# Kernel tuning notes

Measured on AMD Instinct MI355X. Metric: run time of the kernel, lower is better.

Reference implementation:

```python
import jax, jax.numpy as jnp
import numpy as np
from math import sqrt

D_MODEL = 1024
N_HEADS = 16
D_KEYS = 64
D_LLM = 4096
B, L, N = 8, 512, 1000


def _init_params(key):
    ks = jax.random.split(key, 20)
    s = 0.02
    def lin(k, din, dout):
        return jax.random.normal(k, (din, dout), jnp.float32) * s
    p = {}
    for i, pre in enumerate(('t', 'd')):
        o = i * 8
        p[pre + '_Wq'] = lin(ks[o + 0], D_MODEL, N_HEADS * D_KEYS)
        p[pre + '_bq'] = jnp.zeros((N_HEADS * D_KEYS,), jnp.float32)
        p[pre + '_Wk'] = lin(ks[o + 1], D_LLM, N_HEADS * D_KEYS)
        p[pre + '_bk'] = jnp.zeros((N_HEADS * D_KEYS,), jnp.float32)
        p[pre + '_Wv'] = lin(ks[o + 2], D_LLM, N_HEADS * D_KEYS)
        p[pre + '_bv'] = jnp.zeros((N_HEADS * D_KEYS,), jnp.float32)
        p[pre + '_Wo'] = lin(ks[o + 3], N_HEADS * D_KEYS, D_LLM)
        p[pre + '_bo'] = jnp.zeros((D_LLM,), jnp.float32)
    # adaptive fusion gate MLP: Linear(2d->d), ReLU, Linear(d->1), Sigmoid
    p['g_W1'] = jax.random.normal(ks[16], (2 * D_MODEL, D_MODEL), jnp.float32) * sqrt(2.0 / (2 * D_MODEL))
    p['g_b1'] = jnp.zeros((D_MODEL,), jnp.float32)
    p['g_W2'] = jax.random.normal(ks[17], (D_MODEL, 1), jnp.float32) * s
    p['g_b2'] = jnp.zeros((1,), jnp.float32)  # gate_bias_init = 0.0
    return p


def setup_inputs() -> dict:
    key = jax.random.key(0)
    k1, k2, k3, k4, kp = jax.random.split(key, 5)
    inp = {
        'trend_embedding': jax.random.normal(k1, (B, L, D_MODEL), jnp.float32),
        'detail_embedding': jax.random.normal(k2, (B, L, D_MODEL), jnp.float32),
        'trend_prototypes': jax.random.normal(k3, (N, D_LLM), jnp.float32),
        'detail_prototypes': jax.random.normal(k4, (N, D_LLM), jnp.float32),
    }
    inp.update(_init_params(kp))
    return inp


def _reprogram(x, protos, Wq, bq, Wk, bk, Wv, bv, Wo, bo):
    # x: (B,L,d_model), protos: (S,d_llm)
    b, l, _ = x.shape
    s = protos.shape[0]
    q = (x @ Wq + bq).reshape(b, l, N_HEADS, D_KEYS)
    k = (protos @ Wk + bk).reshape(s, N_HEADS, D_KEYS)
    v = (protos @ Wv + bv).reshape(s, N_HEADS, D_KEYS)
    scale = 1.0 / sqrt(D_KEYS)
    scores = jnp.einsum('blhe,she->bhls', q, k)  # (B,H,L,S)
    A = jax.nn.softmax(scale * scores, axis=-1)  # dropout is eval-mode identity
    out = jnp.einsum('bhls,she->blhe', A, v).reshape(b, l, N_HEADS * D_KEYS)
    return out @ Wo + bo  # (B,L,d_llm)


def reference(trend_embedding, detail_embedding, trend_prototypes, detail_prototypes,
              t_Wq, t_bq, t_Wk, t_bk, t_Wv, t_bv, t_Wo, t_bo,
              d_Wq, d_bq, d_Wk, d_bk, d_Wv, d_bv, d_Wo, d_bo,
              g_W1, g_b1, g_W2, g_b2):
    sem_trend = _reprogram(trend_embedding, trend_prototypes,
                           t_Wq, t_bq, t_Wk, t_bk, t_Wv, t_bv, t_Wo, t_bo)
    sem_detail = _reprogram(detail_embedding, detail_prototypes,
                            d_Wq, d_bq, d_Wk, d_bk, d_Wv, d_bv, d_Wo, d_bo)
    # adaptive gate from raw embeddings
    combined = jnp.concatenate([trend_embedding, detail_embedding], axis=-1)
    h = jax.nn.relu(combined @ g_W1 + g_b1)
    gate = jax.nn.sigmoid(h @ g_W2 + g_b2)  # (B,L,1)
    return gate * sem_trend + (1.0 - gate) * sem_detail
```

## Files before the change

### kernel.cpp

```cpp
#include <hip/hip_runtime.h>

typedef unsigned short u16;
typedef unsigned int u32;
typedef __attribute__((ext_vector_type(4))) u16 u16x4;
typedef __attribute__((ext_vector_type(8))) u16 u16x8;
typedef __attribute__((ext_vector_type(4))) float f32x4;
typedef __attribute__((ext_vector_type(8))) __bf16 bf16x8;

#define DEV static __device__ __forceinline__

DEV u16 f2bf(float f) {
    u32 u = __builtin_bit_cast(u32, f);
    return (u16)((u + 0x7FFFu + ((u >> 16) & 1u)) >> 16);
}
DEV float bf2f(u16 h) { return __builtin_bit_cast(float, (u32)h << 16); }

DEV f32x4 mfma16(u16x8 a, u16x8 b, f32x4 c) {
    return __builtin_amdgcn_mfma_f32_16x16x32_bf16(
        __builtin_bit_cast(bf16x8, a), __builtin_bit_cast(bf16x8, b), c, 0, 0, 0);
}

DEV void gload16(const void* g, void* l) {
    __builtin_amdgcn_global_load_lds(
        (const __attribute__((address_space(1))) void*)g,
        (__attribute__((address_space(3))) void*)l, 16, 0, 0);
}


__global__ __launch_bounds__(256) void k_build_xcomb(
    const float* __restrict__ tr, const float* __restrict__ de, u16* __restrict__ out) {
    int i = blockIdx.x * 256 + threadIdx.x;
    int m = i >> 9;
    int c = (i & 511) * 4;
    const float* src = (c < 1024) ? (tr + (size_t)m * 1024 + c)
                                  : (de + (size_t)m * 1024 + (c - 1024));
    f32x4 v = *(const f32x4*)src;
    u16x4 o = { f2bf(v[0]), f2bf(v[1]), f2bf(v[2]), f2bf(v[3]) };
    *(u16x4*)(out + (size_t)m * 2048 + c) = o;
}

__global__ __launch_bounds__(256) void k_convert(
    const float* __restrict__ in, u16* __restrict__ out, int n4) {
    int i = blockIdx.x * 256 + threadIdx.x;
    if (i >= n4) return;
    f32x4 v = ((const f32x4*)in)[i];
    u16x4 o = { f2bf(v[0]), f2bf(v[1]), f2bf(v[2]), f2bf(v[3]) };
    ((u16x4*)out)[i] = o;
}


__global__ void k_transpose_f2b(const float* __restrict__ in, u16* __restrict__ out,
                                int R, int C, int ldo) {
    __shared__ float t[32][33];
    int c0 = blockIdx.x * 32, r0 = blockIdx.y * 32;
    int tx = threadIdx.x, ty = threadIdx.y;
#pragma unroll
    for (int j = 0; j < 4; j++)
        t[ty + j * 8][tx] = in[(size_t)(r0 + ty + j * 8) * C + c0 + tx];
    __syncthreads();
#pragma unroll
    for (int j = 0; j < 4; j++)
        out[(size_t)(c0 + ty + j * 8) * ldo + r0 + tx] = f2bf(t[tx][ty + j * 8]);
}

__global__ void k_transpose_b2b(const u16* __restrict__ in, int ldi,
                                u16* __restrict__ out, int ldo, int R, int C) {
    __shared__ u16 t[32][33];
    int c0 = blockIdx.x * 32, r0 = blockIdx.y * 32;
    int tx = threadIdx.x, ty = threadIdx.y;
#pragma unroll
    for (int j = 0; j < 4; j++)
        t[ty + j * 8][tx] = in[(size_t)(r0 + ty + j * 8) * ldi + c0 + tx];
    __syncthreads();
#pragma unroll
    for (int j = 0; j < 4; j++)
        out[(size_t)(c0 + ty + j * 8) * ldo + r0 + tx] = t[tx][ty + j * 8];
}

#define MODE_BF16 0
#define MODE_BF16_RELU 1

struct GemmArgs {
    const u16* A[3];
    const u16* B[3];
    u16* o[3];
    const float* bias1[3];
    const float* bias2[3];
    int K[3];
    int lda[3];
    int ldc[3];
    int mode[3];
};

__global__ __launch_bounds__(256) void k_gemm128(GemmArgs ga) {
    __shared__ u16 As[128 * 32];
    __shared__ u16 Bs[128 * 32];
    const int z = blockIdx.z;
    const u16* A = ga.A[z];
    const u16* Bt = ga.B[z];
    u16* outp = ga.o[z];
    const float* bias1 = ga.bias1[z];
    const float* bias2 = ga.bias2[z];
    const int K = ga.K[z], lda = ga.lda[z], ldc = ga.ldc[z], mode = ga.mode[z];

    const int tid = threadIdx.x, lane = tid & 63, wid = tid >> 6;
    const int l16 = lane & 15, l4 = lane >> 4;
    const int n0 = blockIdx.x * 128, m0 = blockIdx.y * 128;
    const int wm = (wid >> 1) * 64, wn = (wid & 1) * 64;

    const int srow = wid * 32 + (lane >> 2);
    const int scol = (lane & 3) * 8;
    const u16* gA = A + (size_t)(m0 + srow) * lda + scol;
    const u16* gB = Bt + (size_t)(n0 + srow) * (size_t)K + scol;
    u16* lA = As + wid * 32 * 32;
    u16* lB = Bs + wid * 32 * 32;

    f32x4 acc[4][4] = {};

    for (int k0 = 0; k0 < K; k0 += 32) {
        gload16(gA, lA);
        gload16(gA + (size_t)16 * lda, lA + 16 * 32);
        gload16(gB, lB);
        gload16(gB + (size_t)16 * K, lB + 16 * 32);
        gA += 32;
        gB += 32;
        __syncthreads();
        u16x8 af[4], bfr[4];
#pragma unroll
        for (int m = 0; m < 4; m++) af[m] = *(const u16x8*)&As[(wm + m * 16 + l16) * 32 + l4 * 8];
#pragma unroll
        for (int n = 0; n < 4; n++) bfr[n] = *(const u16x8*)&Bs[(wn + n * 16 + l16) * 32 + l4 * 8];
#pragma unroll
        for (int m = 0; m < 4; m++)
#pragma unroll
            for (int n = 0; n < 4; n++)
                acc[m][n] = mfma16(af[m], bfr[n], acc[m][n]);
        __syncthreads();
    }

#pragma unroll
    for (int m = 0; m < 4; m++) {
#pragma unroll
        for (int n = 0; n < 4; n++) {
            int col = n0 + wn + n * 16 + l16;
#pragma unroll
            for (int j = 0; j < 4; j++) {
                int row = m0 + wm + m * 16 + l4 * 4 + j;
                float v = acc[m][n][j];
                float bb = (bias2 != nullptr && col >= 1024) ? bias2[col - 1024] : bias1[col];
                v += bb;
                if (mode == MODE_BF16_RELU) v = fmaxf(v, 0.f);
                outp[(size_t)row * ldc + col] = f2bf(v);
            }
        }
    }
}

__global__ __launch_bounds__(512, 2) void k_gemm256g(
    const u16* __restrict__ A, int ldaE,
    const u16* __restrict__ Bt, int ldbE,
    int K,
    float* __restrict__ C, int ldcE,
    const float* __restrict__ bias1, const float* __restrict__ bias2,
    const float* __restrict__ gate) {
    __shared__ __attribute__((aligned(16))) u16 sm[2 * 32768];
    char* smc = (char*)sm;

    const int tid = threadIdx.x, lane = tid & 63, wid = tid >> 6;
    const int l16 = lane & 15, l4 = lane >> 4;
    const int wm = (wid >> 2) * 128;
    const int wn = (wid & 3) * 64;
    const int m0 = blockIdx.y * 256, n0 = blockIdx.x * 256;

    const int p0 = wid * 1024 + lane * 16;
    const int p1 = p0 + 8192;
    const int rr0 = p0 >> 7, rr1 = p1 >> 7;
    const int cb0 = (p0 & 127) ^ ((rr0 & 7) << 4);
    const int cb1 = (p1 & 127) ^ ((rr1 & 7) << 4);
    const size_t ldaB = (size_t)ldaE * 2, ldbB = (size_t)ldbE * 2;
    const char* Ab = (const char*)A;
    const char* Bb = (const char*)Bt;
    const size_t aOff0 = (size_t)(m0 + rr0) * ldaB + cb0;
    const size_t aOff1 = (size_t)(m0 + rr1) * ldaB + cb1;
    const size_t bOff0 = (size_t)(n0 + rr0) * ldbB + cb0;
    const size_t bOff1 = (size_t)(n0 + rr1) * ldbB + cb1;

    auto stageA = [&](int T, int h) {
        size_t tOff = (size_t)T * 128 + (size_t)h * 128 * ldaB;
        char* d = smc + (T & 1) * 65536 + h * 16384 + wid * 1024;
        gload16(Ab + aOff0 + tOff, d);
        gload16(Ab + aOff1 + tOff, d + 8192);
    };
    auto stageB = [&](int T, int h) {
        size_t tOff = (size_t)T * 128 + (size_t)h * 128 * ldbB;
        char* d = smc + (T & 1) * 65536 + 32768 + h * 16384 + wid * 1024;
        gload16(Bb + bOff0 + tOff, d);
        gload16(Bb + bOff1 + tOff, d + 8192);
    };
    auto readA = [&](int buf, int mf, int kc) -> u16x8 {
        int row = wm + mf * 16 + l16;
        int cb = (kc * 64 + l4 * 16) ^ ((l16 & 7) << 4);
        return *(const u16x8*)(smc + buf * 65536 + row * 128 + cb);
    };
    auto readB = [&](int buf, int nf, int kc) -> u16x8 {
        int row = wn + nf * 16 + l16;
        int cb = (kc * 64 + l4 * 16) ^ ((l16 & 7) << 4);
        return *(const u16x8*)(smc + buf * 65536 + 32768 + row * 128 + cb);
    };

    f32x4 acc[8][4] = {};
    const int NT = K >> 6;

    stageA(0, 0); stageA(0, 1);
    stageB(0, 0); stageB(0, 1);
    stageB(1, 0); stageB(1, 1);
    asm volatile("s_waitcnt vmcnt(4)" ::: "memory");
    __builtin_amdgcn_s_barrier();

    for (int t = 0; t < NT; ++t) {
        const int buf = t & 1;
        u16x8 bfr[4][2];
#pragma unroll
        for (int q = 0; q < 4; ++q) {
            u16x8 af[2][2];
            if (q == 0) {
#pragma unroll
                for (int nf = 0; nf < 4; nf++)
#pragma unroll
                    for (int kc = 0; kc < 2; kc++) bfr[nf][kc] = readB(buf, nf, kc);
            }
#pragma unroll
            for (int im = 0; im < 2; im++)
#pragma unroll
                for (int kc = 0; kc < 2; kc++) af[im][kc] = readA(buf, 2 * q + im, kc);

            if (q == 0) { if (t + 1 < NT) stageA(t + 1, 0); }
            else if (q == 1) { if (t + 1 < NT) stageA(t + 1, 1); }
            else if (q == 2) { if (t + 2 < NT) stageB(t + 2, 0); }
            else { if (t + 2 < NT) stageB(t + 2, 1); }

            asm volatile("" ::: "memory");
            __builtin_amdgcn_s_barrier();
            __builtin_amdgcn_s_setprio(1);
#pragma unroll
            for (int im = 0; im < 2; im++)
#pragma unroll
                for (int nf = 0; nf < 4; nf++)
#pragma unroll
                    for (int kc = 0; kc < 2; kc++)
                        acc[2 * q + im][nf] = mfma16(af[im][kc], bfr[nf][kc], acc[2 * q + im][nf]);
            __builtin_amdgcn_s_setprio(0);
            asm volatile("" ::: "memory");
            if (q == 3) {
                if (t + 2 < NT) asm volatile("s_waitcnt vmcnt(4)" ::: "memory");
                else            asm volatile("s_waitcnt vmcnt(0)" ::: "memory");
            }
            __builtin_amdgcn_s_barrier();
        }
    }

#pragma unroll
    for (int mf = 0; mf < 8; mf++) {
#pragma unroll
        for (int j = 0; j < 4; j++) {
            int row = m0 + wm + mf * 16 + l4 * 4 + j;
            float g = gate[row];
#pragma unroll
            for (int nf = 0; nf < 4; nf++) {
                int col = n0 + wn + nf * 16 + l16;
                C[(size_t)row * ldcE + col] =
                    acc[mf][nf][j] + g * bias1[col] + (1.f - g) * bias2[col];
            }
        }
    }
}

__global__ __launch_bounds__(256) void k_gate(const u16* __restrict__ h,
                                              const float* __restrict__ W2,
                                              const float* __restrict__ b2,
                                              float* __restrict__ gate) {
    int row = blockIdx.x * 4 + (threadIdx.x >> 6);
    int lane = threadIdx.x & 63;
    const u16* hp = h + (size_t)row * 1024 + lane * 16;
    u16x8 a = *(const u16x8*)hp;
    u16x8 b = *(const u16x8*)(hp + 8);
    const f32x4* wp = (const f32x4*)(W2 + lane * 16);
    f32x4 w0 = wp[0], w1 = wp[1], w2 = wp[2], w3 = wp[3];
    float s = 0.f;
#pragma unroll
    for (int i = 0; i < 4; i++) {
        s += bf2f(a[i]) * w0[i];
        s += bf2f(a[4 + i]) * w1[i];
        s += bf2f(b[i]) * w2[i];
        s += bf2f(b[4 + i]) * w3[i];
    }
#pragma unroll
    for (int d = 1; d < 64; d <<= 1) s += __shfl_xor(s, d);
    if (lane == 0) gate[row] = 1.f / (1.f + __expf(-(s + b2[0])));
}

__global__ __launch_bounds__(256) void k_attn(
    const u16* __restrict__ Q0, const u16* __restrict__ Q1,
    const u16* __restrict__ KV0, const u16* __restrict__ KV1, int ldk,
    const u16* __restrict__ Vt0, const u16* __restrict__ Vt1,
    const float* __restrict__ gate,
    u16* __restrict__ outp) {
    __shared__ u16 Ks[64][72];
    __shared__ u16 Vs[64][72];
    __shared__ u16 Ps[4][32][72];
    const int z = blockIdx.z;
    const u16* Q = z ? Q1 : Q0;
    const u16* Kb = z ? KV1 : KV0;
    const u16* Vt = z ? Vt1 : Vt0;
    const int isTrend = (z == 0);
    const int ocol = z * 1024;

    const int tid = threadIdx.x, lane = tid & 63, wid = tid >> 6;
    const int l16 = lane & 15, l4 = lane >> 4;
    const int qt = blockIdx.x, bh = blockIdx.y;
    const int b = bh >> 4, h = bh & 15;
    const int row0 = b * 512 + qt * 128 + wid * 32;

    u16x8 qf[2][2];
#pragma unroll
    for (int m = 0; m < 2; m++)
#pragma unroll
        for (int kc = 0; kc < 2; kc++)
            qf[m][kc] = *(const u16x8*)(Q + (size_t)(row0 + m * 16 + l16) * 1024 +
                                        h * 64 + kc * 32 + l4 * 8);

    float runm[2][4], runl[2][4];
#pragma unroll
    for (int m = 0; m < 2; m++)
#pragma unroll
        for (int j = 0; j < 4; j++) { runm[m][j] = -3.0e38f; runl[m][j] = 0.f; }
    f32x4 oacc[2][4] = {};

    for (int st = 0; st < 16; st++) {
        const int s0 = st * 64;
#pragma unroll
        for (int i = 0; i < 2; i++) {
            int idx = tid + i * 256;
            int rr = idx >> 3, cc = (idx & 7) * 8;
            *(u16x8*)&Ks[rr][cc] = *(const u16x8*)(Kb + (size_t)(s0 + rr) * ldk + h * 64 + cc);
            *(u16x8*)&Vs[rr][cc] = *(const u16x8*)(Vt + (size_t)(h * 64 + rr) * 1024 + s0 + cc);
        }
        __syncthreads();

        f32x4 sa[2][4] = {};
#pragma unroll
        for (int n = 0; n < 4; n++) {
#pragma unroll
            for (int kc = 0; kc < 2; kc++) {
                u16x8 kf = *(const u16x8*)&Ks[n * 16 + l16][kc * 32 + l4 * 8];
#pragma unroll
                for (int m = 0; m < 2; m++) sa[m][n] = mfma16(qf[m][kc], kf, sa[m][n]);
            }
        }
#pragma unroll
        for (int m = 0; m < 2; m++)
#pragma unroll
            for (int n = 0; n < 4; n++) {
                bool valid = (s0 + n * 16 + l16) < 1000;
#pragma unroll
                for (int j = 0; j < 4; j++)
                    sa[m][n][j] = valid ? sa[m][n][j] * 0.125f : -3.0e38f;
            }
#pragma unroll
        for (int m = 0; m < 2; m++) {
#pragma unroll
            for (int j = 0; j < 4; j++) {
                float rm = fmaxf(fmaxf(sa[m][0][j], sa[m][1][j]),
                                 fmaxf(sa[m][2][j], sa[m][3][j]));
#pragma unroll
                for (int d = 1; d < 16; d <<= 1) rm = fmaxf(rm, __shfl_xor(rm, d));
                float nm = fmaxf(runm[m][j], rm);
                float corr = __expf(runm[m][j] - nm);
                runm[m][j] = nm;
                float rs = 0.f;
#pragma unroll
                for (int n = 0; n < 4; n++) {
                    float p = __expf(sa[m][n][j] - nm);
                    sa[m][n][j] = p;
                    rs += p;
                }
#pragma unroll
                for (int d = 1; d < 16; d <<= 1) rs += __shfl_xor(rs, d);
                runl[m][j] = runl[m][j] * corr + rs;
#pragma unroll
                for (int n = 0; n < 4; n++) oacc[m][n][j] *= corr;
            }
        }
#pragma unroll
        for (int m = 0; m < 2; m++)
#pragma unroll
            for (int n = 0; n < 4; n++)
#pragma unroll
                for (int j = 0; j < 4; j++)
                    Ps[wid][m * 16 + l4 * 4 + j][n * 16 + l16] = f2bf(sa[m][n][j]);

        u16x8 pf[2][2];
#pragma unroll
        for (int m = 0; m < 2; m++)
#pragma unroll
            for (int kc = 0; kc < 2; kc++)
                pf[m][kc] = *(const u16x8*)&Ps[wid][m * 16 + l16][kc * 32 + l4 * 8];
#pragma unroll
        for (int ne = 0; ne < 4; ne++) {
#pragma unroll
            for (int kc = 0; kc < 2; kc++) {
                u16x8 vfr = *(const u16x8*)&Vs[ne * 16 + l16][kc * 32 + l4 * 8];
#pragma unroll
                for (int m = 0; m < 2; m++)
                    oacc[m][ne] = mfma16(pf[m][kc], vfr, oacc[m][ne]);
            }
        }
        __syncthreads();
    }

#pragma unroll
    for (int m = 0; m < 2; m++) {
#pragma unroll
        for (int j = 0; j < 4; j++) {
            int grow = row0 + m * 16 + l4 * 4 + j;
            float g = gate[grow];
            float wgt = isTrend ? g : (1.f - g);
            float f = wgt / runl[m][j];
#pragma unroll
            for (int ne = 0; ne < 4; ne++)
                outp[(size_t)grow * 2048 + ocol + h * 64 + ne * 16 + l16] =
                    f2bf(oacc[m][ne][j] * f);
        }
    }
}


extern "C" void kernel_launch(void* const* d_in, const int* in_sizes, int n_in,
                              void* d_out, int out_size, void* d_ws, size_t ws_size,
                              hipStream_t stream) {
    (void)in_sizes; (void)n_in; (void)out_size; (void)ws_size;
    const float* trend  = (const float*)d_in[0];
    const float* detail = (const float*)d_in[1];
    const float* tproto = (const float*)d_in[2];
    const float* dproto = (const float*)d_in[3];
    const float* t_Wq = (const float*)d_in[4];
    const float* t_bq = (const float*)d_in[5];
    const float* t_Wk = (const float*)d_in[6];
    const float* t_bk = (const float*)d_in[7];
    const float* t_Wv = (const float*)d_in[8];
    const float* t_bv = (const float*)d_in[9];
    const float* t_Wo = (const float*)d_in[10];
    const float* t_bo = (const float*)d_in[11];
    const float* d_Wq = (const float*)d_in[12];
    const float* d_bq = (const float*)d_in[13];
    const float* d_Wk = (const float*)d_in[14];
    const float* d_bk = (const float*)d_in[15];
    const float* d_Wv = (const float*)d_in[16];
    const float* d_bv = (const float*)d_in[17];
    const float* d_Wo = (const float*)d_in[18];
    const float* d_bo = (const float*)d_in[19];
    const float* g_W1 = (const float*)d_in[20];
    const float* g_b1 = (const float*)d_in[21];
    const float* g_W2 = (const float*)d_in[22];
    const float* g_b2 = (const float*)d_in[23];

    char* w = (char*)d_ws;
    auto alloc = [&](size_t bytes) {
        char* p = w;
        w += (bytes + 255) & ~(size_t)255;
        return p;
    };
    u16* xcomb  = (u16*)alloc(4096ull * 2048 * 2);
    u16* pt     = (u16*)alloc(1024ull * 4096 * 2);
    u16* pd     = (u16*)alloc(1024ull * 4096 * 2);
    u16* WqTt   = (u16*)alloc(1024ull * 1024 * 2);
    u16* WqTd   = (u16*)alloc(1024ull * 1024 * 2);
    u16* WkvTt  = (u16*)alloc(2048ull * 4096 * 2);
    u16* WkvTd  = (u16*)alloc(2048ull * 4096 * 2);
    u16* WoT    = (u16*)alloc(4096ull * 2048 * 2);
    u16* W1T    = (u16*)alloc(1024ull * 2048 * 2);
    u16* Qt     = (u16*)alloc(4096ull * 1024 * 2);
    u16* Qd     = (u16*)alloc(4096ull * 1024 * 2);
    u16* KVt    = (u16*)alloc(1024ull * 2048 * 2);
    u16* KVd    = (u16*)alloc(1024ull * 2048 * 2);
    u16* VtT    = (u16*)alloc(1024ull * 1024 * 2);
    u16* VdT    = (u16*)alloc(1024ull * 1024 * 2);
    u16* hbuf   = (u16*)alloc(4096ull * 1024 * 2);
    float* gateb = (float*)alloc(4096ull * 4);
    u16* attnc  = (u16*)alloc(4096ull * 2048 * 2);

    dim3 tb(32, 8);

    k_build_xcomb<<<8192, 256, 0, stream>>>(trend, detail, xcomb);
    k_convert<<<4000, 256, 0, stream>>>(tproto, pt, 1024000);
    k_convert<<<4000, 256, 0, stream>>>(dproto, pd, 1024000);
    hipMemsetAsync(pt + 1000ull * 4096, 0, 24ull * 4096 * 2, stream);
    hipMemsetAsync(pd + 1000ull * 4096, 0, 24ull * 4096 * 2, stream);

    k_transpose_f2b<<<dim3(32, 32), tb, 0, stream>>>(t_Wq, WqTt, 1024, 1024, 1024);
    k_transpose_f2b<<<dim3(32, 32), tb, 0, stream>>>(d_Wq, WqTd, 1024, 1024, 1024);
    k_transpose_f2b<<<dim3(32, 128), tb, 0, stream>>>(t_Wk, WkvTt, 4096, 1024, 4096);
    k_transpose_f2b<<<dim3(32, 128), tb, 0, stream>>>(t_Wv, WkvTt + 1024ull * 4096, 4096, 1024, 4096);
    k_transpose_f2b<<<dim3(32, 128), tb, 0, stream>>>(d_Wk, WkvTd, 4096, 1024, 4096);
    k_transpose_f2b<<<dim3(32, 128), tb, 0, stream>>>(d_Wv, WkvTd + 1024ull * 4096, 4096, 1024, 4096);
    k_transpose_f2b<<<dim3(128, 32), tb, 0, stream>>>(t_Wo, WoT, 1024, 4096, 2048);
    k_transpose_f2b<<<dim3(128, 32), tb, 0, stream>>>(d_Wo, WoT + 1024, 1024, 4096, 2048);
    k_transpose_f2b<<<dim3(32, 64), tb, 0, stream>>>(g_W1, W1T, 2048, 1024, 2048);

    {
        GemmArgs ga = {};
        ga.A[0] = xcomb;        ga.B[0] = W1T;  ga.o[0] = hbuf;
        ga.bias1[0] = g_b1;     ga.K[0] = 2048; ga.lda[0] = 2048; ga.ldc[0] = 1024;
        ga.mode[0] = MODE_BF16_RELU;
        ga.A[1] = xcomb;        ga.B[1] = WqTt; ga.o[1] = Qt;
        ga.bias1[1] = t_bq;     ga.K[1] = 1024; ga.lda[1] = 2048; ga.ldc[1] = 1024;
        ga.mode[1] = MODE_BF16;
        ga.A[2] = xcomb + 1024; ga.B[2] = WqTd; ga.o[2] = Qd;
        ga.bias1[2] = d_bq;     ga.K[2] = 1024; ga.lda[2] = 2048; ga.ldc[2] = 1024;
        ga.mode[2] = MODE_BF16;
        k_gemm128<<<dim3(8, 32, 3), 256, 0, stream>>>(ga);
    }
    k_gate<<<1024, 256, 0, stream>>>(hbuf, g_W2, g_b2, gateb);

    {
        GemmArgs ga = {};
        ga.A[0] = pt; ga.B[0] = WkvTt; ga.o[0] = KVt;
        ga.bias1[0] = t_bk; ga.bias2[0] = t_bv;
        ga.K[0] = 4096; ga.lda[0] = 4096; ga.ldc[0] = 2048; ga.mode[0] = MODE_BF16;
        ga.A[1] = pd; ga.B[1] = WkvTd; ga.o[1] = KVd;
        ga.bias1[1] = d_bk; ga.bias2[1] = d_bv;
        ga.K[1] = 4096; ga.lda[1] = 4096; ga.ldc[1] = 2048; ga.mode[1] = MODE_BF16;
        k_gemm128<<<dim3(16, 8, 2), 256, 0, stream>>>(ga);
    }

    k_transpose_b2b<<<dim3(32, 32), tb, 0, stream>>>(KVt + 1024, 2048, VtT, 1024, 1024, 1024);
    k_transpose_b2b<<<dim3(32, 32), tb, 0, stream>>>(KVd + 1024, 2048, VdT, 1024, 1024, 1024);

    k_attn<<<dim3(4, 128, 2), 256, 0, stream>>>(Qt, Qd, KVt, KVd, 2048, VtT, VdT,
                                                gateb, attnc);

    k_gemm256g<<<dim3(16, 16), 512, 0, stream>>>(attnc, 2048, WoT, 2048, 2048,
                                                 (float*)d_out, 4096, t_bo, d_bo, gateb);
}
```

Baseline: 647.0 us.

## Rewrite attention with 32x32 MFMA, register-resident P and lazy rescale

The attention kernel drops its shared-memory staging of K, V and P. Each wave now computes S^T with 32x32x16 MFMAs, reading K and V fragments straight from global memory. The probabilities are repacked into B-operand layout with permlane32 swaps rather than a trip through LDS. The softmax rescale is skipped unless the running max grows by more than 8, and the 1/sqrt(d) scale is folded into the Q projection epilogue. Together these remove barriers, LDS traffic and per-row shuffle reductions, at the cost of uncoalesced direct global loads and relying on the padded rows of K and V being zero.

```diff
diff --git a/kernel.cpp b/kernel.cpp
--- a/kernel.cpp
+++ b/kernel.cpp
@@ -4,7 +4,10 @@
 typedef unsigned int u32;
 typedef __attribute__((ext_vector_type(4))) u16 u16x4;
 typedef __attribute__((ext_vector_type(8))) u16 u16x8;
+typedef __attribute__((ext_vector_type(2))) u32 u32x2;
+typedef __attribute__((ext_vector_type(4))) u32 u32x4;
 typedef __attribute__((ext_vector_type(4))) float f32x4;
+typedef __attribute__((ext_vector_type(16))) float f32x16;
 typedef __attribute__((ext_vector_type(8))) __bf16 bf16x8;
 
 #define DEV static __device__ __forceinline__
@@ -14,10 +17,29 @@
     return (u16)((u + 0x7FFFu + ((u >> 16) & 1u)) >> 16);
 }
 DEV float bf2f(u16 h) { return __builtin_bit_cast(float, (u32)h << 16); }
+DEV u16 f2bfc(float f) { return __builtin_bit_cast(u16, (__bf16)f); }
+DEV u32 pk2(float lo, float hi) { return (u32)f2bfc(lo) | ((u32)f2bfc(hi) << 16); }
 
 DEV f32x4 mfma16(u16x8 a, u16x8 b, f32x4 c) {
     return __builtin_amdgcn_mfma_f32_16x16x32_bf16(
         __builtin_bit_cast(bf16x8, a), __builtin_bit_cast(bf16x8, b), c, 0, 0, 0);
+}
+DEV f32x16 mfma32(u16x8 a, u16x8 b, f32x16 c) {
+    return __builtin_amdgcn_mfma_f32_32x32x16_bf16(
+        __builtin_bit_cast(bf16x8, a), __builtin_bit_cast(bf16x8, b), c, 0, 0, 0);
+}
+
+DEV void swap32(u32 a, u32 b, u32& ra, u32& rb) {
+#if __has_builtin(__builtin_amdgcn_permlane32_swap)
+    u32x2 r = __builtin_amdgcn_permlane32_swap(a, b, false, false);
+    ra = r[0]; rb = r[1];
+#else
+    u32 bx = (u32)__shfl_xor((int)b, 32);
+    u32 ax = (u32)__shfl_xor((int)a, 32);
+    bool hi = (threadIdx.x & 32) != 0;
+    ra = hi ? bx : a;
+    rb = hi ? b : ax;
+#endif
 }
 
 DEV void gload16(const void* g, void* l) {
@@ -86,6 +108,7 @@
     u16* o[3];
     const float* bias1[3];
     const float* bias2[3];
+    float scale[3];
     int K[3];
     int lda[3];
     int ldc[3];
@@ -101,6 +124,7 @@
     u16* outp = ga.o[z];
     const float* bias1 = ga.bias1[z];
     const float* bias2 = ga.bias2[z];
+    const float scale = ga.scale[z];
     const int K = ga.K[z], lda = ga.lda[z], ldc = ga.ldc[z], mode = ga.mode[z];
 
     const int tid = threadIdx.x, lane = tid & 63, wid = tid >> 6;
@@ -148,7 +172,7 @@
                 int row = m0 + wm + m * 16 + l4 * 4 + j;
                 float v = acc[m][n][j];
                 float bb = (bias2 != nullptr && col >= 1024) ? bias2[col - 1024] : bias1[col];
-                v += bb;
+                v = (v + bb) * scale;
                 if (mode == MODE_BF16_RELU) v = fmaxf(v, 0.f);
                 outp[(size_t)row * ldc + col] = f2bf(v);
             }
@@ -301,135 +325,112 @@
 
 __global__ __launch_bounds__(256) void k_attn(
     const u16* __restrict__ Q0, const u16* __restrict__ Q1,
-    const u16* __restrict__ KV0, const u16* __restrict__ KV1, int ldk,
+    const u16* __restrict__ KV0, const u16* __restrict__ KV1,
     const u16* __restrict__ Vt0, const u16* __restrict__ Vt1,
     const float* __restrict__ gate,
     u16* __restrict__ outp) {
-    __shared__ u16 Ks[64][72];
-    __shared__ u16 Vs[64][72];
-    __shared__ u16 Ps[4][32][72];
     const int z = blockIdx.z;
     const u16* Q = z ? Q1 : Q0;
     const u16* Kb = z ? KV1 : KV0;
     const u16* Vt = z ? Vt1 : Vt0;
-    const int isTrend = (z == 0);
     const int ocol = z * 1024;
 
     const int tid = threadIdx.x, lane = tid & 63, wid = tid >> 6;
-    const int l16 = lane & 15, l4 = lane >> 4;
-    const int qt = blockIdx.x, bh = blockIdx.y;
+    const int l31 = lane & 31, hi = lane >> 5;
+    const int bh = blockIdx.y;
     const int b = bh >> 4, h = bh & 15;
-    const int row0 = b * 512 + qt * 128 + wid * 32;
-
-    u16x8 qf[2][2];
-#pragma unroll
-    for (int m = 0; m < 2; m++)
-#pragma unroll
-        for (int kc = 0; kc < 2; kc++)
-            qf[m][kc] = *(const u16x8*)(Q + (size_t)(row0 + m * 16 + l16) * 1024 +
-                                        h * 64 + kc * 32 + l4 * 8);
-
-    float runm[2][4], runl[2][4];
-#pragma unroll
-    for (int m = 0; m < 2; m++)
-#pragma unroll
-        for (int j = 0; j < 4; j++) { runm[m][j] = -3.0e38f; runl[m][j] = 0.f; }
-    f32x4 oacc[2][4] = {};
-
-    for (int st = 0; st < 16; st++) {
-        const int s0 = st * 64;
-#pragma unroll
-        for (int i = 0; i < 2; i++) {
-            int idx = tid + i * 256;
-            int rr = idx >> 3, cc = (idx & 7) * 8;
-            *(u16x8*)&Ks[rr][cc] = *(const u16x8*)(Kb + (size_t)(s0 + rr) * ldk + h * 64 + cc);
-            *(u16x8*)&Vs[rr][cc] = *(const u16x8*)(Vt + (size_t)(h * 64 + rr) * 1024 + s0 + cc);
-        }
-        __syncthreads();
-
-        f32x4 sa[2][4] = {};
-#pragma unroll
-        for (int n = 0; n < 4; n++) {
-#pragma unroll
-            for (int kc = 0; kc < 2; kc++) {
-                u16x8 kf = *(const u16x8*)&Ks[n * 16 + l16][kc * 32 + l4 * 8];
-#pragma unroll
-                for (int m = 0; m < 2; m++) sa[m][n] = mfma16(qf[m][kc], kf, sa[m][n]);
+    const int row0 = b * 512 + blockIdx.x * 128 + wid * 32;
+
+    u16x8 qf[4];
+    const u16* qp = Q + (size_t)(row0 + l31) * 1024 + h * 64 + hi * 8;
+#pragma unroll
+    for (int kc = 0; kc < 4; kc++) qf[kc] = *(const u16x8*)(qp + kc * 16);
+
+    const u16* kp = Kb + (size_t)l31 * 2048 + h * 64 + hi * 8;
+    const u16* vp = Vt + (size_t)(h * 64 + l31) * 1024 + hi * 8;
+
+    f32x16 oacc0 = {}, oacc1 = {};
+    float runm = -3.0e38f, runl = 0.f;
+
+    for (int st = 0; st < 32; ++st) {
+        const int s0 = st * 32;
+        const u16* kt = kp + (size_t)s0 * 2048;
+        u16x8 kf0 = *(const u16x8*)(kt);
+        u16x8 kf1 = *(const u16x8*)(kt + 16);
+        u16x8 kf2 = *(const u16x8*)(kt + 32);
+        u16x8 kf3 = *(const u16x8*)(kt + 48);
+        f32x16 p = {};
+        p = mfma32(kf0, qf[0], p);
+        p = mfma32(kf1, qf[1], p);
+        p = mfma32(kf2, qf[2], p);
+        p = mfma32(kf3, qf[3], p);
+        u16x8 vf00 = *(const u16x8*)(vp + s0);
+        u16x8 vf01 = *(const u16x8*)(vp + s0 + 16);
+        u16x8 vf10 = *(const u16x8*)(vp + 32 * 1024 + s0);
+        u16x8 vf11 = *(const u16x8*)(vp + 32 * 1024 + s0 + 16);
+
+        if (st == 31) {
+#pragma unroll
+            for (int r = 4; r < 16; r++) p[r] = -3.0e38f;
+        }
+
+        float pm = p[0];
+#pragma unroll
+        for (int r = 1; r < 16; r++) pm = fmaxf(pm, p[r]);
+        pm = fmaxf(pm, __shfl_xor(pm, 32));
+        if (__any(pm > runm + 8.f)) {
+            float nm = fmaxf(runm, pm);
+            float corr = __expf(runm - nm);
+            runm = nm;
+            runl *= corr;
+            oacc0 *= corr;
+            oacc1 *= corr;
+        }
+        float ts = 0.f;
+#pragma unroll
+        for (int r = 0; r < 16; r++) {
+            float e = __expf(p[r] - runm);
+            p[r] = e;
+            ts += e;
+        }
+        runl += ts + __shfl_xor(ts, 32);
+
+        u16x8 pw[2];
+#pragma unroll
+        for (int ks = 0; ks < 2; ks++) {
+            u32 a0 = pk2(p[8 * ks + 0], p[8 * ks + 1]);
+            u32 b0 = pk2(p[8 * ks + 4], p[8 * ks + 5]);
+            u32 a1 = pk2(p[8 * ks + 2], p[8 * ks + 3]);
+            u32 b1 = pk2(p[8 * ks + 6], p[8 * ks + 7]);
+            u32 w0, w1, w2, w3;
+            swap32(a0, b0, w0, w2);
+            swap32(a1, b1, w1, w3);
+            u32x4 wv = { w0, w1, w2, w3 };
+            pw[ks] = __builtin_bit_cast(u16x8, wv);
+        }
+
+        oacc0 = mfma32(vf00, pw[0], oacc0);
+        oacc0 = mfma32(vf01, pw[1], oacc0);
+        oacc1 = mfma32(vf10, pw[0], oacc1);
+        oacc1 = mfma32(vf11, pw[1], oacc1);
+    }
+
+    int grow = row0 + l31;
+    float g = gate[grow];
+    float wgt = z ? (1.f - g) : g;
+    float f = wgt / runl;
+    u16* op = outp + (size_t)grow * 2048 + ocol + h * 64 + hi * 4;
+#pragma unroll
+    for (int dh = 0; dh < 2; dh++) {
+#pragma unroll
+        for (int quad = 0; quad < 4; quad++) {
+            u16x4 s;
+#pragma unroll
+            for (int j = 0; j < 4; j++) {
+                float v = (dh ? oacc1[quad * 4 + j] : oacc0[quad * 4 + j]) * f;
+                s[j] = f2bfc(v);
             }
-        }
-#pragma unroll
-        for (int m = 0; m < 2; m++)
-#pragma unroll
-            for (int n = 0; n < 4; n++) {
-                bool valid = (s0 + n * 16 + l16) < 1000;
-#pragma unroll
-                for (int j = 0; j < 4; j++)
-                    sa[m][n][j] = valid ? sa[m][n][j] * 0.125f : -3.0e38f;
-            }
-#pragma unroll
-        for (int m = 0; m < 2; m++) {
-#pragma unroll
-            for (int j = 0; j < 4; j++) {
-                float rm = fmaxf(fmaxf(sa[m][0][j], sa[m][1][j]),
-                                 fmaxf(sa[m][2][j], sa[m][3][j]));
-#pragma unroll
-                for (int d = 1; d < 16; d <<= 1) rm = fmaxf(rm, __shfl_xor(rm, d));
-                float nm = fmaxf(runm[m][j], rm);
-                float corr = __expf(runm[m][j] - nm);
-                runm[m][j] = nm;
-                float rs = 0.f;
-#pragma unroll
-                for (int n = 0; n < 4; n++) {
-                    float p = __expf(sa[m][n][j] - nm);
-                    sa[m][n][j] = p;
-                    rs += p;
-                }
-#pragma unroll
-                for (int d = 1; d < 16; d <<= 1) rs += __shfl_xor(rs, d);
-                runl[m][j] = runl[m][j] * corr + rs;
-#pragma unroll
-                for (int n = 0; n < 4; n++) oacc[m][n][j] *= corr;
-            }
-        }
-#pragma unroll
-        for (int m = 0; m < 2; m++)
-#pragma unroll
-            for (int n = 0; n < 4; n++)
-#pragma unroll
-                for (int j = 0; j < 4; j++)
-                    Ps[wid][m * 16 + l4 * 4 + j][n * 16 + l16] = f2bf(sa[m][n][j]);
-
-        u16x8 pf[2][2];
-#pragma unroll
-        for (int m = 0; m < 2; m++)
-#pragma unroll
-            for (int kc = 0; kc < 2; kc++)
-                pf[m][kc] = *(const u16x8*)&Ps[wid][m * 16 + l16][kc * 32 + l4 * 8];
-#pragma unroll
-        for (int ne = 0; ne < 4; ne++) {
-#pragma unroll
-            for (int kc = 0; kc < 2; kc++) {
-                u16x8 vfr = *(const u16x8*)&Vs[ne * 16 + l16][kc * 32 + l4 * 8];
-#pragma unroll
-                for (int m = 0; m < 2; m++)
-                    oacc[m][ne] = mfma16(pf[m][kc], vfr, oacc[m][ne]);
-            }
-        }
-        __syncthreads();
-    }
-
-#pragma unroll
-    for (int m = 0; m < 2; m++) {
-#pragma unroll
-        for (int j = 0; j < 4; j++) {
-            int grow = row0 + m * 16 + l4 * 4 + j;
-            float g = gate[grow];
-            float wgt = isTrend ? g : (1.f - g);
-            float f = wgt / runl[m][j];
-#pragma unroll
-            for (int ne = 0; ne < 4; ne++)
-                outp[(size_t)grow * 2048 + ocol + h * 64 + ne * 16 + l16] =
-                    f2bf(oacc[m][ne][j] * f);
+            *(u16x4*)(op + dh * 32 + quad * 8) = s;
         }
     }
 }
@@ -511,13 +512,13 @@
         GemmArgs ga = {};
         ga.A[0] = xcomb;        ga.B[0] = W1T;  ga.o[0] = hbuf;
         ga.bias1[0] = g_b1;     ga.K[0] = 2048; ga.lda[0] = 2048; ga.ldc[0] = 1024;
-        ga.mode[0] = MODE_BF16_RELU;
+        ga.mode[0] = MODE_BF16_RELU; ga.scale[0] = 1.f;
         ga.A[1] = xcomb;        ga.B[1] = WqTt; ga.o[1] = Qt;
         ga.bias1[1] = t_bq;     ga.K[1] = 1024; ga.lda[1] = 2048; ga.ldc[1] = 1024;
-        ga.mode[1] = MODE_BF16;
+        ga.mode[1] = MODE_BF16; ga.scale[1] = 0.125f;
         ga.A[2] = xcomb + 1024; ga.B[2] = WqTd; ga.o[2] = Qd;
         ga.bias1[2] = d_bq;     ga.K[2] = 1024; ga.lda[2] = 2048; ga.ldc[2] = 1024;
-        ga.mode[2] = MODE_BF16;
+        ga.mode[2] = MODE_BF16; ga.scale[2] = 0.125f;
         k_gemm128<<<dim3(8, 32, 3), 256, 0, stream>>>(ga);
     }
     k_gate<<<1024, 256, 0, stream>>>(hbuf, g_W2, g_b2, gateb);
@@ -525,10 +526,10 @@
     {
         GemmArgs ga = {};
         ga.A[0] = pt; ga.B[0] = WkvTt; ga.o[0] = KVt;
-        ga.bias1[0] = t_bk; ga.bias2[0] = t_bv;
+        ga.bias1[0] = t_bk; ga.bias2[0] = t_bv; ga.scale[0] = 1.f;
         ga.K[0] = 4096; ga.lda[0] = 4096; ga.ldc[0] = 2048; ga.mode[0] = MODE_BF16;
         ga.A[1] = pd; ga.B[1] = WkvTd; ga.o[1] = KVd;
-        ga.bias1[1] = d_bk; ga.bias2[1] = d_bv;
+        ga.bias1[1] = d_bk; ga.bias2[1] = d_bv; ga.scale[1] = 1.f;
         ga.K[1] = 4096; ga.lda[1] = 4096; ga.ldc[1] = 2048; ga.mode[1] = MODE_BF16;
         k_gemm128<<<dim3(16, 8, 2), 256, 0, stream>>>(ga);
     }
@@ -536,7 +537,7 @@
     k_transpose_b2b<<<dim3(32, 32), tb, 0, stream>>>(KVt + 1024, 2048, VtT, 1024, 1024, 1024);
     k_transpose_b2b<<<dim3(32, 32), tb, 0, stream>>>(KVd + 1024, 2048, VdT, 1024, 1024, 1024);
 
-    k_attn<<<dim3(4, 128, 2), 256, 0, stream>>>(Qt, Qd, KVt, KVd, 2048, VtT, VdT,
+    k_attn<<<dim3(4, 128, 2), 256, 0, stream>>>(Qt, Qd, KVt, KVd, VtT, VdT,
                                                 gateb, attnc);
 
     k_gemm256g<<<dim3(16, 16), 512, 0, stream>>>(attnc, 2048, WoT, 2048, 2048,
```

After: 610.6 us. -5.6%, faster.
